# Kernel optimization log

Measured on AMD Instinct MI355X. Metric: run time of the kernel, lower is better.

The kernel has to match this reference:

```python
import jax, jax.numpy as jnp
import numpy as np

D_MODEL = 512
N_HEAD = 8
D_HEAD = D_MODEL // N_HEAD
S = 192   # qlen; must equal bsz for this module's shapes to be consistent
B = 192   # bsz (== rlen, since pos_seq = inputs[0, :, 0])
EPS = 1e-5
SCALE = 1.0 / (D_HEAD ** 0.5)


def _layer_norm(x, g, b):
    mu = jnp.mean(x, axis=-1, keepdims=True)
    var = jnp.mean(jnp.square(x - mu), axis=-1, keepdims=True)
    return (x - mu) * jax.lax.rsqrt(var + EPS) * g + b


def _rel_shift(x):
    # x: (qlen, rlen, bsz, n_head) -- TransformerXL rel_shift memory trick
    q, r, b, n = x.shape
    zero_pad = jnp.zeros((q, 1, b, n), dtype=x.dtype)
    x_padded = jnp.concatenate([zero_pad, x], axis=1)       # (q, r+1, b, n)
    x_padded = x_padded.reshape(r + 1, q, b, n)
    return x_padded[1:].reshape(q, r, b, n)


def setup_inputs() -> dict:
    key = jax.random.key(0)
    ks = jax.random.split(key, 8)
    s = 0.02
    inputs = jax.random.normal(ks[0], (S, B, D_MODEL), dtype=jnp.float32)
    return {
        "inputs": inputs,
        "ln1_g": jnp.ones((D_MODEL,), jnp.float32),
        "ln1_b": jnp.zeros((D_MODEL,), jnp.float32),
        "ln2_g": jnp.ones((D_MODEL,), jnp.float32),
        "ln2_b": jnp.zeros((D_MODEL,), jnp.float32),
        "W_qkv": jax.random.normal(ks[1], (3 * D_MODEL, D_MODEL), jnp.float32) * s,
        "W_r": jax.random.normal(ks[2], (D_MODEL, D_MODEL), jnp.float32) * s,
        "W_o": jax.random.normal(ks[3], (D_MODEL, D_MODEL), jnp.float32) * s,
        "r_w_bias": jax.random.normal(ks[4], (N_HEAD, D_HEAD), jnp.float32) * s,
        "r_r_bias": jax.random.normal(ks[5], (N_HEAD, D_HEAD), jnp.float32) * s,
    }


def reference(inputs, ln1_g, ln1_b, ln2_g, ln2_b, W_qkv, W_r, W_o, r_w_bias, r_r_bias):
    # PositionalEmbedding over pos_seq = inputs[0, :, 0]  (length bsz)
    pos_seq = inputs[0, :, 0]                                   # (B,)
    inv_freq = 1.0 / (10000.0 ** (jnp.arange(0, D_MODEL, 2, dtype=jnp.float32) / D_MODEL))
    sin_inp = pos_seq[:, None] * inv_freq[None, :]              # (B, d/2)
    pos_emb = jnp.concatenate([jnp.sin(sin_inp), jnp.cos(sin_inp)], axis=-1)  # (R=B, d)

    x = _layer_norm(inputs, ln1_g, ln1_b)                       # outer LN
    h = _layer_norm(x, ln2_g, ln2_b)                            # MHA-internal LN

    w_heads = jnp.einsum('sbd,ed->sbe', h, W_qkv)               # (S, B, 3*d_model)
    q, k, v = jnp.split(w_heads, 3, axis=-1)
    q = q.reshape(S, B, N_HEAD, D_HEAD)
    k = k.reshape(S, B, N_HEAD, D_HEAD)
    v = v.reshape(S, B, N_HEAD, D_HEAD)
    r_head_k = (pos_emb @ W_r.T).reshape(B, N_HEAD, D_HEAD)     # (R, H, D)

    AC = jnp.einsum('ibnd,jbnd->ijbn', q + r_w_bias, k)         # content term
    BD = jnp.einsum('ibnd,jnd->ijbn', q + r_r_bias, r_head_k)   # rel-pos term
    BD = _rel_shift(BD)

    attn_score = (AC + BD) * SCALE                              # (S, S, B, H)
    attn_prob = jax.nn.softmax(attn_score, axis=1)

    attn_vec = jnp.einsum('ijbn,jbnd->ibnd', attn_prob, v)      # (S, B, H, D)
    attn_vec = attn_vec.reshape(S, B, D_MODEL)
    return attn_vec @ W_o.T                                     # (S, B, d_model)
```

## Files before the change

### kernel.cpp

```cpp
#include <hip/hip_runtime.h>
#include <math.h>

#define SQ 192
#define BB 192
#define DM 512
#define NH 8
#define DH 64
#define NEPS 1e-5f
#define ASCALE 0.125f

typedef __bf16 bf16x8 __attribute__((ext_vector_type(8)));
typedef float f32x4 __attribute__((ext_vector_type(4)));
typedef unsigned short u16x8 __attribute__((ext_vector_type(8)));

__device__ __forceinline__ void gload16(const unsigned short* g, unsigned short* l) {
  __builtin_amdgcn_global_load_lds(
      (const __attribute__((address_space(1))) void*)g,
      (__attribute__((address_space(3))) void*)l, 16, 0, 0);
}
__device__ __forceinline__ unsigned short f2b(float x) {
  union { float f; unsigned u; } c; c.f = x;
  return (unsigned short)((c.u + 0x7fffu + ((c.u >> 16) & 1u)) >> 16);
}
__device__ __forceinline__ float f2bf(float x) {
  union { float f; unsigned u; } c; c.f = x;
  c.u = (c.u + 0x7fffu + ((c.u >> 16) & 1u)) & 0xffff0000u;
  return c.f;
}
__device__ __forceinline__ float b2f(unsigned short h) {
  union { unsigned u; float f; } c; c.u = ((unsigned)h) << 16;
  return c.f;
}
__device__ __forceinline__ bf16x8 u2b8(u16x8 v) {
  union { u16x8 u; bf16x8 b; } c; c.u = v; return c.b;
}

__global__ __launch_bounds__(128) void ln2_kernel(
    const float* __restrict__ inp, const float* __restrict__ g1, const float* __restrict__ b1,
    const float* __restrict__ g2, const float* __restrict__ b2,
    unsigned short* __restrict__ hbhi) {
  const int R = blockIdx.x;
  const int s = R / BB;
  const int b = R % BB;
  const int t = threadIdx.x;
  const float4 v = reinterpret_cast<const float4*>(inp + (size_t)R * DM)[t];
  float sum  = v.x + v.y + v.z + v.w;
  float sum2 = v.x*v.x + v.y*v.y + v.z*v.z + v.w*v.w;
  #pragma unroll
  for (int o = 32; o >= 1; o >>= 1) { sum += __shfl_xor(sum, o); sum2 += __shfl_xor(sum2, o); }
  __shared__ float red[2][2];
  const int wv = t >> 6;
  if ((t & 63) == 0) { red[0][wv] = sum; red[1][wv] = sum2; }
  __syncthreads();
  sum = red[0][0] + red[0][1]; sum2 = red[1][0] + red[1][1];
  float mu = sum * (1.0f / DM);
  float var = sum2 * (1.0f / DM) - mu * mu;
  float rstd = rsqrtf(var + NEPS);
  const float4 G1 = reinterpret_cast<const float4*>(g1)[t];
  const float4 B1 = reinterpret_cast<const float4*>(b1)[t];
  float4 x;
  x.x = (v.x - mu) * rstd * G1.x + B1.x;
  x.y = (v.y - mu) * rstd * G1.y + B1.y;
  x.z = (v.z - mu) * rstd * G1.z + B1.z;
  x.w = (v.w - mu) * rstd * G1.w + B1.w;
  sum  = x.x + x.y + x.z + x.w;
  sum2 = x.x*x.x + x.y*x.y + x.z*x.z + x.w*x.w;
  #pragma unroll
  for (int o = 32; o >= 1; o >>= 1) { sum += __shfl_xor(sum, o); sum2 += __shfl_xor(sum2, o); }
  __syncthreads();
  if ((t & 63) == 0) { red[0][wv] = sum; red[1][wv] = sum2; }
  __syncthreads();
  sum = red[0][0] + red[0][1]; sum2 = red[1][0] + red[1][1];
  mu = sum * (1.0f / DM);
  var = sum2 * (1.0f / DM) - mu * mu;
  rstd = rsqrtf(var + NEPS);
  const float4 G2 = reinterpret_cast<const float4*>(g2)[t];
  const float4 B2 = reinterpret_cast<const float4*>(b2)[t];
  ushort4 hh;
  hh.x = f2b((x.x - mu) * rstd * G2.x + B2.x);
  hh.y = f2b((x.y - mu) * rstd * G2.y + B2.y);
  hh.z = f2b((x.z - mu) * rstd * G2.z + B2.z);
  hh.w = f2b((x.w - mu) * rstd * G2.w + B2.w);
  *reinterpret_cast<ushort4*>(hbhi + ((size_t)b * SQ + s) * DM + t * 4) = hh;
}

__global__ void posemb_kernel(const float* __restrict__ inp, float* __restrict__ pe) {
  const int idx = blockIdx.x * 256 + threadIdx.x;
  if (idx >= BB * DM) return;
  const int b = idx >> 9;
  const int d = idx & 511;
  const float ps = inp[(size_t)b * DM];
  const int i = (d < 256) ? d : (d - 256);
  const float invf = expf(-9.210340371976184f * (float)i * (1.0f / 256.0f));
  const float a = ps * invf;
  pe[idx] = (d < 256) ? sinf(a) : cosf(a);
}

__global__ __launch_bounds__(256) void rhk_kernel(
    const float* __restrict__ pe, const float* __restrict__ Wr, unsigned short* __restrict__ rhkb) {
  __shared__ __align__(16) float pr[DM];
  const int j = blockIdx.x;
  const int e = blockIdx.y * 256 + threadIdx.x;
  for (int d = threadIdx.x; d < DM; d += 256) pr[d] = pe[(size_t)j * DM + d];
  __syncthreads();
  const float4* w4 = reinterpret_cast<const float4*>(Wr + (size_t)e * DM);
  const float4* p4 = reinterpret_cast<const float4*>(pr);
  float acc = 0.f;
  #pragma unroll 8
  for (int d4 = 0; d4 < DM / 4; ++d4) {
    const float4 a = p4[d4];
    const float4 w = w4[d4];
    acc += a.x*w.x + a.y*w.y + a.z*w.z + a.w*w.w;
  }
  rhkb[(size_t)j * DM + e] = f2b(acc);
}

__global__ void convhi_kernel(const float* __restrict__ src, unsigned short* __restrict__ dst, int nel) {
  const int i = blockIdx.x * 256 + threadIdx.x;
  if (i < nel) dst[i] = f2b(src[i]);
}

__global__ __launch_bounds__(256, 2) void gemm_mfma(
    const unsigned short* __restrict__ Ahi, const unsigned short* __restrict__ Alo,
    const unsigned short* __restrict__ Bp,
    unsigned short* __restrict__ Chi, float* __restrict__ Cf, int N, int mode, int ksteps) {
  __shared__ __align__(16) unsigned short As[2][128][64];
  __shared__ __align__(16) unsigned short Bs[2][128][64];
  const int tid = threadIdx.x;
  const int nwg = gridDim.x * gridDim.y;
  int flat = blockIdx.y * gridDim.x + blockIdx.x;
  flat = (flat & 7) * (nwg >> 3) + (flat >> 3);
  const int bm = (flat / gridDim.x) * 128;
  const int bn = (flat % gridDim.x) * 128;
  const int lane = tid & 63, wv = tid >> 6;
  const int wm = (wv >> 1) << 6, wn = (wv & 1) << 6;
  const int fr = lane & 15, q4 = lane >> 4;
  const int srow_ = tid >> 3, sl = tid & 7;

  f32x4 acc[4][4];
  #pragma unroll
  for (int mt = 0; mt < 4; ++mt)
    #pragma unroll
    for (int nt = 0; nt < 4; ++nt) acc[mt][nt] = (f32x4){0.f, 0.f, 0.f, 0.f};

  auto STAGE = [&](int buf, int k0) {
    const unsigned short* Ap = (k0 < 512) ? Ahi : Alo;
    const int kk = k0 & 511;
    #pragma unroll
    for (int it = 0; it < 4; ++it) {
      const int row = it * 32 + srow_;
      const int sp = (sl ^ (row & 7)) << 3;
      gload16(Ap + (size_t)(bm + row) * 512 + kk + sp, &As[buf][row][sl << 3]);
      gload16(Bp + (size_t)(bn + row) * 512 + kk + sp, &Bs[buf][row][sl << 3]);
    }
  };

  STAGE(0, 0);
  __syncthreads();
  int buf = 0;
  for (int step = 0; step < ksteps; ++step) {
    if (step < ksteps - 1) STAGE(buf ^ 1, (step + 1) * 64);
    bf16x8 a[4][2], bb[4][2];
    #pragma unroll
    for (int mt = 0; mt < 4; ++mt)
      #pragma unroll
      for (int kc = 0; kc < 2; ++kc) {
        const int ra = wm + mt * 16 + fr;
        a[mt][kc]  = *reinterpret_cast<const bf16x8*>(&As[buf][ra][((((kc << 2) | q4) ^ (ra & 7)) << 3)]);
        const int rb = wn + mt * 16 + fr;
        bb[mt][kc] = *reinterpret_cast<const bf16x8*>(&Bs[buf][rb][((((kc << 2) | q4) ^ (rb & 7)) << 3)]);
      }
    #pragma unroll
    for (int mt = 0; mt < 4; ++mt)
      #pragma unroll
      for (int nt = 0; nt < 4; ++nt) {
        acc[mt][nt] = __builtin_amdgcn_mfma_f32_16x16x32_bf16(a[mt][0], bb[nt][0], acc[mt][nt], 0, 0, 0);
        acc[mt][nt] = __builtin_amdgcn_mfma_f32_16x16x32_bf16(a[mt][1], bb[nt][1], acc[mt][nt], 0, 0, 0);
      }
    __syncthreads();
    buf ^= 1;
  }
  const int crow0 = bm + wm + (q4 << 2);
  const int ccol0 = bn + wn + fr;
  if (mode == 0) {
    #pragma unroll
    for (int mt = 0; mt < 4; ++mt)
      #pragma unroll
      for (int r = 0; r < 4; ++r) {
        const size_t rr = crow0 + mt * 16 + r;
        #pragma unroll
        for (int nt = 0; nt < 4; ++nt)
          Chi[rr * 1536 + ccol0 + nt * 16] = f2b(acc[mt][nt][r]);
      }
  } else {
    #pragma unroll
    for (int mt = 0; mt < 4; ++mt)
      #pragma unroll
      for (int r = 0; r < 4; ++r) {
        const int rr = crow0 + mt * 16 + r;
        const size_t orow = (size_t)(rr % SQ) * BB + (rr / SQ);
        #pragma unroll
        for (int nt = 0; nt < 4; ++nt)
          Cf[orow * N + ccol0 + nt * 16] = acc[mt][nt][r];
      }
  }
}

#define Q0   0
#define R0   12288
#define K0   24576
#define U0   36864
#define VT0  0
#define OH0  0
#define OL0  15360
#define UPIT 200

__global__ __launch_bounds__(768) void attn_mfma(
    const unsigned short* __restrict__ qkvhi,
    const unsigned short* __restrict__ rhkb,
    const float* __restrict__ rwb, const float* __restrict__ rrb,
    unsigned short* __restrict__ avhi, unsigned short* __restrict__ avlo, int b0) {
  __shared__ __align__(16) unsigned short lds[75264];
  const int bid = blockIdx.x;
  const int n = bid & 7, bl = bid >> 3;
  const int tid = threadIdx.x;
  const int lane = tid & 63, wv = tid >> 6;
  const int fr = lane & 15, q4 = lane >> 4;
  const int wrow = (wv / 6) * 96 + (wv % 6) * 16;
  const size_t rin = (size_t)bl * SQ;
  const size_t rout = (size_t)(b0 + bl) * SQ;

  #pragma unroll
  for (int it = 0; it < 2; ++it) {
    const int u = it * 768 + tid;
    const int row = u >> 3, sl = u & 7, sp = (sl ^ (row & 7)) << 3;
    gload16(qkvhi + (rin + row) * 1536 + n * 64 + sp, &lds[Q0 + (row << 6) + (sl << 3)]);
    gload16(rhkb + (size_t)row * 512 + n * 64 + sp, &lds[R0 + (row << 6) + (sl << 3)]);
    gload16(qkvhi + (rin + row) * 1536 + 512 + n * 64 + sp, &lds[K0 + (row << 6) + (sl << 3)]);
  }
  const int vj = tid % 192, vdg = tid / 192;
  u16x8 vreg[2];
  #pragma unroll
  for (int c = 0; c < 2; ++c)
    vreg[c] = *reinterpret_cast<const u16x8*>(qkvhi + (rin + vj) * 1536 + 1024 + n * 64 + vdg * 16 + c * 8);
  __syncthreads();

  bf16x8 aw[2], ar[2];
  {
    const int row_l = wrow + fr;
    #pragma unroll
    for (int kc = 0; kc < 2; ++kc) {
      const u16x8 qraw = *reinterpret_cast<const u16x8*>(
          &lds[Q0 + (row_l << 6) + ((((kc << 2) | q4) ^ (row_l & 7)) << 3)]);
      u16x8 wv_, rv_;
      #pragma unroll
      for (int e = 0; e < 8; ++e) {
        const int k = kc * 32 + (q4 << 3) + e;
        const float qf = b2f(qraw[e]);
        wv_[e] = f2b(qf + rwb[n * 64 + k]);
        rv_[e] = f2b(qf + rrb[n * 64 + k]);
      }
      aw[kc] = u2b8(wv_); ar[kc] = u2b8(rv_);
    }
  }

  f32x4 acc[12], uacc[12];
  #pragma unroll
  for (int nt = 0; nt < 12; ++nt) {
    acc[nt] = (f32x4){0.f, 0.f, 0.f, 0.f};
    uacc[nt] = (f32x4){0.f, 0.f, 0.f, 0.f};
  }
  #pragma unroll
  for (int nt = 0; nt < 12; ++nt) {
    #pragma unroll
    for (int kc = 0; kc < 2; ++kc) {
      const int r_ = nt * 16 + fr;
      const int sp = ((((kc << 2) | q4) ^ (r_ & 7)) << 3);
      const bf16x8 bk = *reinterpret_cast<const bf16x8*>(&lds[K0 + (r_ << 6) + sp]);
      const bf16x8 br = *reinterpret_cast<const bf16x8*>(&lds[R0 + (r_ << 6) + sp]);
      acc[nt]  = __builtin_amdgcn_mfma_f32_16x16x32_bf16(aw[kc], bk, acc[nt], 0, 0, 0);
      uacc[nt] = __builtin_amdgcn_mfma_f32_16x16x32_bf16(ar[kc], br, uacc[nt], 0, 0, 0);
    }
  }
  #pragma unroll
  for (int nt = 0; nt < 12; ++nt)
    #pragma unroll
    for (int r = 0; r < 4; ++r) {
      const int i_l = wrow + (q4 << 2) + r;
      lds[U0 + i_l * UPIT + nt * 16 + fr] = f2b(uacc[nt][r]);
    }
  __syncthreads();

  #pragma unroll
  for (int c = 0; c < 2; ++c)
    #pragma unroll
    for (int e = 0; e < 8; ++e)
      lds[VT0 + (vdg * 16 + c * 8 + e) * UPIT + vj] = vreg[c][e];

  float linv[4];
  #pragma unroll
  for (int r = 0; r < 4; ++r) {
    const int i = wrow + (q4 << 2) + r;
    float ls = 0.f;
    #pragma unroll
    for (int nt = 0; nt < 12; ++nt) {
      const int j = nt * 16 + fr;
      const int t = j + 191 - i;
      const bool wrap = (t >= 193);
      const int tm = wrap ? t - 193 : t;
      const bool valid = (t != 192);
      const int rowu = i + (wrap ? 1 : 0);
      const float uv = b2f(lds[U0 + rowu * UPIT + (valid ? tm : 0)]);
      const float sr = acc[nt][r] + (valid ? uv : 0.f);
      const float p = f2bf(__expf(sr * ASCALE));
      ls += p;
      acc[nt][r] = p;
    }
    #pragma unroll
    for (int o = 1; o <= 8; o <<= 1) ls += __shfl_xor(ls, o);
    linv[r] = 1.0f / ls;
  }
  __syncthreads();

  #pragma unroll
  for (int nt = 0; nt < 12; ++nt)
    #pragma unroll
    for (int r = 0; r < 4; ++r) {
      const int i_l = wrow + (q4 << 2) + r;
      lds[U0 + i_l * UPIT + nt * 16 + fr] = f2b(acc[nt][r]);
    }
  __syncthreads();

  f32x4 o2[4];
  #pragma unroll
  for (int nt = 0; nt < 4; ++nt) o2[nt] = (f32x4){0.f, 0.f, 0.f, 0.f};
  #pragma unroll
  for (int kc = 0; kc < 6; ++kc) {
    const bf16x8 pa = *reinterpret_cast<const bf16x8*>(
        &lds[U0 + (wrow + fr) * UPIT + kc * 32 + (q4 << 3)]);
    #pragma unroll
    for (int nt = 0; nt < 4; ++nt) {
      const bf16x8 vb = *reinterpret_cast<const bf16x8*>(
          &lds[VT0 + (nt * 16 + fr) * UPIT + kc * 32 + (q4 << 3)]);
      o2[nt] = __builtin_amdgcn_mfma_f32_16x16x32_bf16(pa, vb, o2[nt], 0, 0, 0);
    }
  }
  __syncthreads();

  #pragma unroll
  for (int nt = 0; nt < 4; ++nt)
    #pragma unroll
    for (int r = 0; r < 4; ++r) {
      const int i_l = wrow + (q4 << 2) + r;
      const int d = nt * 16 + fr;
      const float v = o2[nt][r] * linv[r];
      lds[OH0 + i_l * 80 + d] = f2b(v);
      lds[OL0 + i_l * 80 + d] = f2b(v - f2bf(v));
    }
  __syncthreads();
  #pragma unroll
  for (int it = 0; it < 2; ++it) {
    const int u = it * 768 + tid;
    const int row = u >> 3, sl = u & 7;
    const size_t gbase = (rout + row) * 512 + n * 64 + sl * 8;
    *reinterpret_cast<u16x8*>(avhi + gbase) = *reinterpret_cast<const u16x8*>(&lds[OH0 + row * 80 + sl * 8]);
    *reinterpret_cast<u16x8*>(avlo + gbase) = *reinterpret_cast<const u16x8*>(&lds[OL0 + row * 80 + sl * 8]);
  }
}

extern "C" void kernel_launch(void* const* d_in, const int* in_sizes, int n_in,
                              void* d_out, int out_size, void* d_ws, size_t ws_size,
                              hipStream_t stream) {
  const float* inp   = (const float*)d_in[0];
  const float* ln1_g = (const float*)d_in[1];
  const float* ln1_b = (const float*)d_in[2];
  const float* ln2_g = (const float*)d_in[3];
  const float* ln2_b = (const float*)d_in[4];
  const float* Wqkv  = (const float*)d_in[5];
  const float* Wr    = (const float*)d_in[6];
  const float* Wo    = (const float*)d_in[7];
  const float* rwb   = (const float*)d_in[8];
  const float* rrb   = (const float*)d_in[9];
  float* out = (float*)d_out;

  const size_t M = (size_t)SQ * BB;
  unsigned short* hbhi = (unsigned short*)d_out;

  const int cands[3] = {192, 96, 48};
  int CB = 48;
  for (int ci = 0; ci < 3; ++ci) {
    const int c = cands[ci];
    const size_t need = (size_t)c * SQ * 1536 * 2
                      + 2 * M * 512 * 2
                      + 1536 * 512 * 2 + 512 * 512 * 2
                      + (size_t)BB * DM * 4 + (size_t)BB * DM * 2;
    if (need <= ws_size) { CB = c; break; }
  }

  char* p = (char*)d_ws;
  unsigned short* qhi  = (unsigned short*)p; p += (size_t)CB * SQ * 1536 * 2;
  unsigned short* avhi = (unsigned short*)p; p += M * 512 * 2;
  unsigned short* avlo = (unsigned short*)p; p += M * 512 * 2;
  unsigned short* Wqb  = (unsigned short*)p; p += (size_t)1536 * 512 * 2;
  unsigned short* Wob  = (unsigned short*)p; p += (size_t)512 * 512 * 2;
  float*          pe   = (float*)p;          p += (size_t)BB * DM * 4;
  unsigned short* rhkb = (unsigned short*)p;

  ln2_kernel<<<SQ * BB, 128, 0, stream>>>(inp, ln1_g, ln1_b, ln2_g, ln2_b, hbhi);
  posemb_kernel<<<(BB * DM + 255) / 256, 256, 0, stream>>>(inp, pe);
  rhk_kernel<<<dim3(BB, DM / 256), 256, 0, stream>>>(pe, Wr, rhkb);
  convhi_kernel<<<(1536 * 512 + 255) / 256, 256, 0, stream>>>(Wqkv, Wqb, 1536 * 512);
  convhi_kernel<<<(512 * 512 + 255) / 256, 256, 0, stream>>>(Wo, Wob, 512 * 512);

  for (int b0 = 0; b0 < BB; b0 += CB) {
    const int Mc = CB * SQ;
    gemm_mfma<<<dim3(1536 / 128, Mc / 128), 256, 0, stream>>>(
        hbhi + (size_t)b0 * SQ * DM, hbhi + (size_t)b0 * SQ * DM, Wqb,
        qhi, nullptr, 1536, 0, 8);
    attn_mfma<<<CB * NH, 768, 0, stream>>>(qhi, rhkb, rwb, rrb, avhi, avlo, b0);
  }

  gemm_mfma<<<dim3(512 / 128, M / 128), 256, 0, stream>>>(
      avhi, avlo, Wob, nullptr, out, 512, 1, 16);
}
```

Measured before the change: 304.0 us.

## Scatter rel-shifted BD into transposed layout, fold scale into Q, merge weight conversions

The relative-shift term is now scattered into a transposed LDS layout when it is stored, so the softmax pass reads four consecutive values with one vector load instead of doing per-element wrap and index math. The attention scale is folded into the biased query before the MFMA, the per-probability bf16 rounding is dropped, a fast reciprocal replaces the division, and one barrier is removed. The two weight-conversion launches are merged into one kernel. Rounding behaviour changes slightly, and the scatter with zeroed diagonal entries must reproduce the rel_shift semantics exactly.

```diff
diff --git a/kernel.cpp b/kernel.cpp
--- a/kernel.cpp
+++ b/kernel.cpp
@@ -12,6 +12,7 @@
 typedef __bf16 bf16x8 __attribute__((ext_vector_type(8)));
 typedef float f32x4 __attribute__((ext_vector_type(4)));
 typedef unsigned short u16x8 __attribute__((ext_vector_type(8)));
+typedef unsigned short u16x4 __attribute__((ext_vector_type(4)));
 
 __device__ __forceinline__ void gload16(const unsigned short* g, unsigned short* l) {
   __builtin_amdgcn_global_load_lds(
@@ -115,9 +116,11 @@
   rhkb[(size_t)j * DM + e] = f2b(acc);
 }
 
-__global__ void convhi_kernel(const float* __restrict__ src, unsigned short* __restrict__ dst, int nel) {
+__global__ void conv2_kernel(const float* __restrict__ wq, const float* __restrict__ wo,
+                             unsigned short* __restrict__ wqb, unsigned short* __restrict__ wob) {
   const int i = blockIdx.x * 256 + threadIdx.x;
-  if (i < nel) dst[i] = f2b(src[i]);
+  if (i < 786432) wqb[i] = f2b(wq[i]);
+  else if (i < 786432 + 262144) wob[i - 786432] = f2b(wo[i - 786432]);
 }
 
 __global__ __launch_bounds__(256, 2) void gemm_mfma(
@@ -227,6 +230,7 @@
   const int lane = tid & 63, wv = tid >> 6;
   const int fr = lane & 15, q4 = lane >> 4;
   const int wrow = (wv / 6) * 96 + (wv % 6) * 16;
+  const int i0q = wrow + (q4 << 2);
   const size_t rin = (size_t)bl * SQ;
   const size_t rout = (size_t)(b0 + bl) * SQ;
 
@@ -238,6 +242,7 @@
     gload16(rhkb + (size_t)row * 512 + n * 64 + sp, &lds[R0 + (row << 6) + (sl << 3)]);
     gload16(qkvhi + (rin + row) * 1536 + 512 + n * 64 + sp, &lds[K0 + (row << 6) + (sl << 3)]);
   }
+  if (tid < 191) lds[U0 + tid * UPIT + tid] = 0;
   const int vj = tid % 192, vdg = tid / 192;
   u16x8 vreg[2];
   #pragma unroll
@@ -257,8 +262,8 @@
       for (int e = 0; e < 8; ++e) {
         const int k = kc * 32 + (q4 << 3) + e;
         const float qf = b2f(qraw[e]);
-        wv_[e] = f2b(qf + rwb[n * 64 + k]);
-        rv_[e] = f2b(qf + rrb[n * 64 + k]);
+        wv_[e] = f2b((qf + rwb[n * 64 + k]) * ASCALE);
+        rv_[e] = f2b((qf + rrb[n * 64 + k]) * ASCALE);
       }
       aw[kc] = u2b8(wv_); ar[kc] = u2b8(rv_);
     }
@@ -283,12 +288,17 @@
     }
   }
   #pragma unroll
-  for (int nt = 0; nt < 12; ++nt)
+  for (int nt = 0; nt < 12; ++nt) {
+    const int t = nt * 16 + fr;
     #pragma unroll
     for (int r = 0; r < 4; ++r) {
-      const int i_l = wrow + (q4 << 2) + r;
-      lds[U0 + i_l * UPIT + nt * 16 + fr] = f2b(uacc[nt][r]);
-    }
+      const int i = i0q + r;
+      const int s = t + i;
+      const int col = (s >= 191) ? i : (i - 1);
+      const int m = (s >= 192) ? (s - 192) : s;
+      if (col >= 0) lds[U0 + m * UPIT + col] = f2b(uacc[nt][r]);
+    }
+  }
   __syncthreads();
 
   #pragma unroll
@@ -297,39 +307,33 @@
     for (int e = 0; e < 8; ++e)
       lds[VT0 + (vdg * 16 + c * 8 + e) * UPIT + vj] = vreg[c][e];
 
+  float ls[4] = {0.f, 0.f, 0.f, 0.f};
+  #pragma unroll
+  for (int nt = 0; nt < 12; ++nt) {
+    const int j = nt * 16 + fr;
+    const int m = (j == 0) ? 191 : (j - 1);
+    const u16x4 uv = *reinterpret_cast<const u16x4*>(&lds[U0 + m * UPIT + i0q]);
+    #pragma unroll
+    for (int r = 0; r < 4; ++r) {
+      const float p = __expf(acc[nt][r] + b2f(uv[r]));
+      ls[r] += p;
+      acc[nt][r] = p;
+    }
+  }
   float linv[4];
   #pragma unroll
   for (int r = 0; r < 4; ++r) {
-    const int i = wrow + (q4 << 2) + r;
-    float ls = 0.f;
-    #pragma unroll
-    for (int nt = 0; nt < 12; ++nt) {
-      const int j = nt * 16 + fr;
-      const int t = j + 191 - i;
-      const bool wrap = (t >= 193);
-      const int tm = wrap ? t - 193 : t;
-      const bool valid = (t != 192);
-      const int rowu = i + (wrap ? 1 : 0);
-      const float uv = b2f(lds[U0 + rowu * UPIT + (valid ? tm : 0)]);
-      const float sr = acc[nt][r] + (valid ? uv : 0.f);
-      const float p = f2bf(__expf(sr * ASCALE));
-      ls += p;
-      acc[nt][r] = p;
-    }
-    #pragma unroll
-    for (int o = 1; o <= 8; o <<= 1) ls += __shfl_xor(ls, o);
-    linv[r] = 1.0f / ls;
+    #pragma unroll
+    for (int o = 1; o <= 8; o <<= 1) ls[r] += __shfl_xor(ls[r], o);
+    linv[r] = __builtin_amdgcn_rcpf(ls[r]);
   }
   __syncthreads();
 
   #pragma unroll
   for (int nt = 0; nt < 12; ++nt)
     #pragma unroll
-    for (int r = 0; r < 4; ++r) {
-      const int i_l = wrow + (q4 << 2) + r;
-      lds[U0 + i_l * UPIT + nt * 16 + fr] = f2b(acc[nt][r]);
-    }
-  __syncthreads();
+    for (int r = 0; r < 4; ++r)
+      lds[U0 + (i0q + r) * UPIT + nt * 16 + fr] = f2b(acc[nt][r]);
 
   f32x4 o2[4];
   #pragma unroll
@@ -351,7 +355,7 @@
   for (int nt = 0; nt < 4; ++nt)
     #pragma unroll
     for (int r = 0; r < 4; ++r) {
-      const int i_l = wrow + (q4 << 2) + r;
+      const int i_l = i0q + r;
       const int d = nt * 16 + fr;
       const float v = o2[nt][r] * linv[r];
       lds[OH0 + i_l * 80 + d] = f2b(v);
@@ -409,8 +413,7 @@
   ln2_kernel<<<SQ * BB, 128, 0, stream>>>(inp, ln1_g, ln1_b, ln2_g, ln2_b, hbhi);
   posemb_kernel<<<(BB * DM + 255) / 256, 256, 0, stream>>>(inp, pe);
   rhk_kernel<<<dim3(BB, DM / 256), 256, 0, stream>>>(pe, Wr, rhkb);
-  convhi_kernel<<<(1536 * 512 + 255) / 256, 256, 0, stream>>>(Wqkv, Wqb, 1536 * 512);
-  convhi_kernel<<<(512 * 512 + 255) / 256, 256, 0, stream>>>(Wo, Wob, 512 * 512);
+  conv2_kernel<<<(786432 + 262144 + 255) / 256, 256, 0, stream>>>(Wqkv, Wo, Wqb, Wob);
 
   for (int b0 = 0; b0 < BB; b0 += CB) {
     const int Mc = CB * SQ;
```

Result: faster. 289.7 us (-4.7%).
